# Performance work log

Measured on AMD Instinct MI355X. Metric: run time of the kernel, lower is better.

The kernel has to match this reference:

```python
import jax, jax.numpy as jnp
import numpy as np

DEPTH = 6
H = 12
D = 768
FF = 4 * D
OUT_INDICES = (2, 5)
EPS = 1e-5


def layernorm(x, g, b):
    m = jnp.mean(x, axis=-1, keepdims=True)
    v = jnp.mean(jnp.square(x - m), axis=-1, keepdims=True)
    return (x - m) * jax.lax.rsqrt(v + EPS) * g + b


def setup_inputs() -> dict:
    key = jax.random.key(0)
    ks = jax.random.split(key, 8)
    B, N = 2, 1024
    s = 0.02
    inp = {
        "x": jax.random.normal(ks[0], (B, N, D), dtype=jnp.float32),
        "rel_bias": jax.random.normal(ks[1], (H, N, N), dtype=jnp.float32),
        "ln1_g": jnp.ones((DEPTH, D), jnp.float32),
        "ln1_b": jnp.zeros((DEPTH, D), jnp.float32),
        "qkv_w": jax.random.normal(ks[2], (DEPTH, D, 3 * D), dtype=jnp.float32) * s,
        "out_w": jax.random.normal(ks[3], (DEPTH, D, D), dtype=jnp.float32) * s,
        "out_b": jnp.zeros((DEPTH, D), jnp.float32),
        "ln2_g": jnp.ones((DEPTH, D), jnp.float32),
        "ln2_b": jnp.zeros((DEPTH, D), jnp.float32),
        "ff1_w": jax.random.normal(ks[4], (DEPTH, D, FF), dtype=jnp.float32) * s,
        "ff1_b": jnp.zeros((DEPTH, FF), jnp.float32),
        "ff2_w": jax.random.normal(ks[5], (DEPTH, FF, D), dtype=jnp.float32) * s,
        "ff2_b": jnp.zeros((DEPTH, D), jnp.float32),
        "lnf_g": jnp.ones((D,), jnp.float32),
        "lnf_b": jnp.zeros((D,), jnp.float32),
    }
    return inp


def reference(x, rel_bias, ln1_g, ln1_b, qkv_w, out_w, out_b, ln2_g, ln2_b,
              ff1_w, ff1_b, ff2_w, ff2_b, lnf_g, lnf_b):
    B, N, Dm = x.shape
    Dh = Dm // H
    scale = Dh ** -0.5
    kside = int(round(N ** 0.5))  # N is a perfect square (patch grid)
    feats = []
    for i in range(DEPTH):
        # --- attention block ---
        h = layernorm(x, ln1_g[i], ln1_b[i])
        qkv = h @ qkv_w[i]                                   # [B,N,3D]
        q, k, v = jnp.split(qkv, 3, axis=-1)
        q = q.reshape(B, N, H, Dh).transpose(0, 2, 1, 3)     # [B,H,N,Dh]
        k = k.reshape(B, N, H, Dh).transpose(0, 2, 1, 3)
        v = v.reshape(B, N, H, Dh).transpose(0, 2, 1, 3)
        scores = jnp.einsum('bhid,bhjd->bhij', q, k) * scale + rel_bias
        attn = jax.nn.softmax(scores, axis=-1)
        o = jnp.einsum('bhij,bhjd->bhid', attn, v)
        o = o.transpose(0, 2, 1, 3).reshape(B, N, Dm)
        x = x + (o @ out_w[i] + out_b[i])
        # --- FFN block ---
        h2 = layernorm(x, ln2_g[i], ln2_b[i])
        ff = jax.nn.gelu(h2 @ ff1_w[i] + ff1_b[i], approximate=False)
        x = x + (ff @ ff2_w[i] + ff2_b[i])
        if i in OUT_INDICES:
            feats.append(x.reshape(B, kside, kside, Dm).transpose(0, 3, 1, 2))
    xf = layernorm(x, lnf_g, lnf_b)
    return (xf, *feats)
```

## Files before the change

### kernel.cpp

```cpp
#include <hip/hip_runtime.h>
#include <hip/hip_bf16.h>

typedef unsigned short ushort_t;
typedef __attribute__((ext_vector_type(8))) __bf16 bf16x8;
typedef __attribute__((ext_vector_type(4))) float f32x4;
typedef __attribute__((ext_vector_type(4))) unsigned int u32x4;

#define DEPTH 6
#define HEADS 12
#define DMODEL 768
#define FFDIM 3072
#define BATCH 2
#define SEQ 1024
#define ROWS (BATCH * SEQ)

static __device__ __forceinline__ ushort_t f2bf(float f) {
  unsigned u = __builtin_bit_cast(unsigned, f);
  u += 0x7fffu + ((u >> 16) & 1u);
  return (ushort_t)(u >> 16);
}

template <int MREP, int NREP, int EPI>
__global__ __launch_bounds__(256) void gemm_bt(
    const ushort_t* __restrict__ A, const ushort_t* __restrict__ Bt,
    int lda, int ldb, int K,
    void* __restrict__ out0, void* __restrict__ out1,
    const float* __restrict__ f0) {
  constexpr int BM = 32 * MREP;
  constexpr int BN = 32 * NREP;
  constexpr int CHA = BM / 32;
  constexpr int CHB = BN / 32;
  __shared__ ushort_t sA[2][BM * 64];
  __shared__ ushort_t sB[2][BN * 64];

  const int tid = threadIdx.x;
  const int lane = tid & 63;
  const int wid = tid >> 6;
  const int wm = wid >> 1, wn = wid & 1;

  const ushort_t* Ab = A + (long)blockIdx.x * BM * lda;
  const ushort_t* Bb = Bt + (long)blockIdx.y * BN * ldb;

  const int srow = lane >> 3;
  const int scol = ((lane & 7) ^ srow) * 8;

  f32x4 acc[MREP][NREP];
#pragma unroll
  for (int m = 0; m < MREP; ++m)
#pragma unroll
    for (int n = 0; n < NREP; ++n) acc[m][n] = (f32x4){0.f, 0.f, 0.f, 0.f};

  const int fr = lane & 15;
  const int kq4 = lane >> 4;

  auto stage_tile = [&](int buf, int t) {
    const int k0 = t * 64;
#pragma unroll
    for (int j = 0; j < CHA; ++j) {
      const int c = wid * CHA + j;
      const ushort_t* src = Ab + (long)(c * 8 + srow) * lda + k0 + scol;
      __builtin_amdgcn_global_load_lds(
          (const __attribute__((address_space(1))) void*)src,
          (__attribute__((address_space(3))) void*)&sA[buf][c * 512], 16, 0, 0);
    }
#pragma unroll
    for (int j = 0; j < CHB; ++j) {
      const int c = wid * CHB + j;
      const ushort_t* src = Bb + (long)(c * 8 + srow) * ldb + k0 + scol;
      __builtin_amdgcn_global_load_lds(
          (const __attribute__((address_space(1))) void*)src,
          (__attribute__((address_space(3))) void*)&sB[buf][c * 512], 16, 0, 0);
    }
  };

  const int nt = K / 64;
  stage_tile(0, 0);
  for (int t = 0; t < nt; ++t) {
    const int cur = t & 1;
    asm volatile("s_waitcnt vmcnt(0)" ::: "memory");
    __builtin_amdgcn_s_barrier();
    if (t + 1 < nt) stage_tile(cur ^ 1, t + 1);
#pragma unroll
    for (int kk = 0; kk < 2; ++kk) {
      bf16x8 af[MREP], bfr[NREP];
#pragma unroll
      for (int m = 0; m < MREP; ++m) {
        const int row = wm * (MREP * 16) + m * 16 + fr;
        const int ch = (kk * 4 + kq4) ^ (row & 7);
        af[m] = *(const bf16x8*)&sA[cur][row * 64 + ch * 8];
      }
#pragma unroll
      for (int n = 0; n < NREP; ++n) {
        const int row = wn * (NREP * 16) + n * 16 + fr;
        const int ch = (kk * 4 + kq4) ^ (row & 7);
        bfr[n] = *(const bf16x8*)&sB[cur][row * 64 + ch * 8];
      }
#pragma unroll
      for (int m = 0; m < MREP; ++m)
#pragma unroll
        for (int n = 0; n < NREP; ++n)
          acc[m][n] = __builtin_amdgcn_mfma_f32_16x16x32_bf16(
              af[m], bfr[n], acc[m][n], 0, 0, 0);
    }
  }

  const long grow0 = (long)blockIdx.x * BM + wm * (MREP * 16);
  const long gcol0 = (long)blockIdx.y * BN + wn * (NREP * 16);
  const int rr = (lane >> 4) * 4;
  const int cc = lane & 15;

#pragma unroll
  for (int m = 0; m < MREP; ++m) {
#pragma unroll
    for (int n = 0; n < NREP; ++n) {
#pragma unroll
      for (int r = 0; r < 4; ++r) {
        long row = grow0 + m * 16 + rr + r;
        long col = gcol0 + n * 16 + cc;
        float c = acc[m][n][r];
        if (EPI == 0) {
          ushort_t bv = f2bf(c);
          if (col < 1536) {
            ((ushort_t*)out0)[row * 2304 + col] = bv;
          } else {
            long h = (col - 1536) >> 6, d = (col - 1536) & 63;
            long b = row >> 10, i = row & 1023;
            ((ushort_t*)out1)[(((b * HEADS) + h) * 64 + d) * 1024 + i] = bv;
          }
        } else if (EPI == 3) {
          long idx = row * DMODEL + col;
          ((float*)out0)[idx] += c + f0[col];
        } else if (EPI == 4) {
          float t = c + f0[col];
          float g = 0.5f * t * (1.0f + erff(t * 0.70710678118f));
          ((ushort_t*)out0)[row * FFDIM + col] = f2bf(g);
        } else if (EPI == 5) {
          long idx = row * DMODEL + col;
          ((float*)out0)[idx] += c + f0[col];
        }
      }
    }
  }
}

__global__ __launch_bounds__(256) void flash_attn(
    const ushort_t* __restrict__ qkv,
    const ushort_t* __restrict__ vt,
    const float* __restrict__ rel,
    ushort_t* __restrict__ o) {
  __shared__ ushort_t sK[2][64 * 64];
  __shared__ ushort_t sV[2][64 * 64];
  __shared__ ushort_t sP[64 * 64];

  const int tid = threadIdx.x;
  const int lane = tid & 63;
  const int wid = tid >> 6;
  const int h = blockIdx.y, b = blockIdx.z;
  const int q0 = blockIdx.x * 64;

  const int fr = lane & 15;
  const int kq4 = lane >> 4;
  const int rr = kq4 * 4;
  const int cc = fr;

  const int srow = lane >> 3;
  const int scol = ((lane & 7) ^ srow) * 8;

  const ushort_t* qbase =
      qkv + (size_t)(b * 1024 + q0 + wid * 16 + fr) * 2304 + h * 64;
  bf16x8 qreg[2];
  qreg[0] = *(const bf16x8*)&qbase[kq4 * 8];
  qreg[1] = *(const bf16x8*)&qbase[32 + kq4 * 8];

  const ushort_t* Kbase = qkv + (size_t)(b * 1024) * 2304 + 768 + h * 64;
  const ushort_t* Vbase = vt + (size_t)((b * HEADS + h) * 64) * 1024;

  f32x4 acc_o[4];
  float m_run[4], l_run[4];
#pragma unroll
  for (int n = 0; n < 4; ++n) acc_o[n] = (f32x4){0.f, 0.f, 0.f, 0.f};
#pragma unroll
  for (int r = 0; r < 4; ++r) { m_run[r] = -1e30f; l_run[r] = 0.f; }

  auto stage_kv = [&](int buf, int t) {
#pragma unroll
    for (int j = 0; j < 2; ++j) {
      const int c = wid * 2 + j;
      const ushort_t* src = Kbase + (size_t)(t * 64 + c * 8 + srow) * 2304 + scol;
      __builtin_amdgcn_global_load_lds(
          (const __attribute__((address_space(1))) void*)src,
          (__attribute__((address_space(3))) void*)&sK[buf][c * 512], 16, 0, 0);
    }
#pragma unroll
    for (int j = 0; j < 2; ++j) {
      const int c = wid * 2 + j;
      const ushort_t* src = Vbase + (size_t)(c * 8 + srow) * 1024 + t * 64 + scol;
      __builtin_amdgcn_global_load_lds(
          (const __attribute__((address_space(1))) void*)src,
          (__attribute__((address_space(3))) void*)&sV[buf][c * 512], 16, 0, 0);
    }
  };

  stage_kv(0, 0);
  for (int t = 0; t < 16; ++t) {
    const int cur = t & 1;
    asm volatile("s_waitcnt vmcnt(0)" ::: "memory");
    __builtin_amdgcn_s_barrier();

    float bias[4][4];
    {
      const float* rb = rel + ((size_t)h << 20) +
                        (size_t)(q0 + wid * 16 + rr) * 1024 + t * 64 + cc;
#pragma unroll
      for (int n = 0; n < 4; ++n)
#pragma unroll
        for (int r = 0; r < 4; ++r) bias[n][r] = rb[(size_t)r * 1024 + n * 16];
    }

    if (t + 1 < 16) stage_kv(cur ^ 1, t + 1);

    f32x4 s[4];
#pragma unroll
    for (int n = 0; n < 4; ++n) s[n] = (f32x4){0.f, 0.f, 0.f, 0.f};
#pragma unroll
    for (int kk = 0; kk < 2; ++kk) {
#pragma unroll
      for (int n = 0; n < 4; ++n) {
        const int row = n * 16 + fr;
        const int ch = (kk * 4 + kq4) ^ (row & 7);
        bf16x8 kf = *(const bf16x8*)&sK[cur][row * 64 + ch * 8];
        s[n] =
            __builtin_amdgcn_mfma_f32_16x16x32_bf16(qreg[kk], kf, s[n], 0, 0, 0);
      }
    }

    float mr[4];
#pragma unroll
    for (int r = 0; r < 4; ++r) mr[r] = -1e30f;
#pragma unroll
    for (int n = 0; n < 4; ++n)
#pragma unroll
      for (int r = 0; r < 4; ++r) {
        float v = s[n][r] * 0.125f + bias[n][r];
        s[n][r] = v;
        mr[r] = fmaxf(mr[r], v);
      }
#pragma unroll
    for (int o_ = 1; o_ < 16; o_ <<= 1)
#pragma unroll
      for (int r = 0; r < 4; ++r) mr[r] = fmaxf(mr[r], __shfl_xor(mr[r], o_));

    float escale[4], psum[4];
#pragma unroll
    for (int r = 0; r < 4; ++r) {
      float mn = fmaxf(m_run[r], mr[r]);
      escale[r] = __expf(m_run[r] - mn);
      m_run[r] = mn;
      psum[r] = 0.f;
    }
#pragma unroll
    for (int n = 0; n < 4; ++n)
#pragma unroll
      for (int r = 0; r < 4; ++r) {
        float p = __expf(s[n][r] - m_run[r]);
        psum[r] += p;
        const int prow = wid * 16 + rr + r;
        const int pcol = n * 16 + cc;
        sP[prow * 64 + (((pcol >> 3) ^ (prow & 7)) << 3) + (pcol & 7)] = f2bf(p);
      }
#pragma unroll
    for (int o_ = 1; o_ < 16; o_ <<= 1)
#pragma unroll
      for (int r = 0; r < 4; ++r) psum[r] += __shfl_xor(psum[r], o_);
#pragma unroll
    for (int r = 0; r < 4; ++r) l_run[r] = l_run[r] * escale[r] + psum[r];

    asm volatile("s_waitcnt lgkmcnt(0)" ::: "memory");
    __builtin_amdgcn_s_barrier();

#pragma unroll
    for (int n = 0; n < 4; ++n)
#pragma unroll
      for (int r = 0; r < 4; ++r) acc_o[n][r] *= escale[r];
#pragma unroll
    for (int kk = 0; kk < 2; ++kk) {
      const int prow = wid * 16 + fr;
      const int pch = (kk * 4 + kq4) ^ (prow & 7);
      bf16x8 pf = *(const bf16x8*)&sP[prow * 64 + pch * 8];
#pragma unroll
      for (int n = 0; n < 4; ++n) {
        const int vrow = n * 16 + fr;
        const int vch = (kk * 4 + kq4) ^ (vrow & 7);
        bf16x8 vf = *(const bf16x8*)&sV[cur][vrow * 64 + vch * 8];
        acc_o[n] =
            __builtin_amdgcn_mfma_f32_16x16x32_bf16(pf, vf, acc_o[n], 0, 0, 0);
      }
    }
  }

  ushort_t* ob = o + (size_t)(b * 1024 + q0 + wid * 16) * 768 + h * 64;
#pragma unroll
  for (int r = 0; r < 4; ++r) {
    const float rinv = 1.f / l_run[r];
#pragma unroll
    for (int n = 0; n < 4; ++n)
      ob[(size_t)(rr + r) * 768 + n * 16 + cc] = f2bf(acc_o[n][r] * rinv);
  }
}

__global__ __launch_bounds__(256) void transpose_cast(
    const float* __restrict__ in, ushort_t* __restrict__ out, int R, int C) {
  __shared__ float t[32][33];
  const float* ip = in + (long)blockIdx.z * R * C;
  ushort_t* op = out + (long)blockIdx.z * R * C;
  int c0 = blockIdx.x * 32, r0 = blockIdx.y * 32;
  int tx = threadIdx.x;
  for (int i = threadIdx.y; i < 32; i += 8)
    t[i][tx] = ip[(long)(r0 + i) * C + c0 + tx];
  __syncthreads();
  for (int i = threadIdx.y; i < 32; i += 8)
    op[(long)(c0 + i) * R + r0 + tx] = f2bf(t[tx][i]);
}

__global__ __launch_bounds__(256) void ln_kernel(
    const float* __restrict__ x, const float* __restrict__ g,
    const float* __restrict__ b, void* __restrict__ out, int out_f32) {
  int row = blockIdx.x;
  int tid = threadIdx.x;
  int lane = tid & 63, wid = tid >> 6;
  const float* xr = x + (long)row * DMODEL;
  float v0 = xr[tid], v1 = xr[tid + 256], v2 = xr[tid + 512];
  float s = v0 + v1 + v2;
  __shared__ float red[8];
  for (int o = 32; o; o >>= 1) s += __shfl_xor(s, o);
  if (!lane) red[wid] = s;
  __syncthreads();
  float mean = (red[0] + red[1] + red[2] + red[3]) * (1.f / 768.f);
  float d0 = v0 - mean, d1 = v1 - mean, d2 = v2 - mean;
  float q = d0 * d0 + d1 * d1 + d2 * d2;
  for (int o = 32; o; o >>= 1) q += __shfl_xor(q, o);
  if (!lane) red[4 + wid] = q;
  __syncthreads();
  float var = (red[4] + red[5] + red[6] + red[7]) * (1.f / 768.f);
  float rs = rsqrtf(var + 1e-5f);
  float y0 = d0 * rs * g[tid] + b[tid];
  float y1 = d1 * rs * g[tid + 256] + b[tid + 256];
  float y2 = d2 * rs * g[tid + 512] + b[tid + 512];
  if (out_f32) {
    float* o_ = (float*)out + (long)row * DMODEL;
    o_[tid] = y0; o_[tid + 256] = y1; o_[tid + 512] = y2;
  } else {
    ushort_t* o_ = (ushort_t*)out + (long)row * DMODEL;
    o_[tid] = f2bf(y0); o_[tid + 256] = f2bf(y1); o_[tid + 512] = f2bf(y2);
  }
}

__global__ __launch_bounds__(256) void feat_kernel(const float* __restrict__ x,
                                                   float* __restrict__ out) {
  __shared__ float t[32][33];
  const float* xp = x + (long)blockIdx.z * SEQ * DMODEL;
  float* op = out + (long)blockIdx.z * DMODEL * SEQ;
  int n0 = blockIdx.x * 32, c0 = blockIdx.y * 32;
  int tx = threadIdx.x;
  for (int i = threadIdx.y; i < 32; i += 8)
    t[i][tx] = xp[(long)(n0 + i) * DMODEL + c0 + tx];
  __syncthreads();
  for (int i = threadIdx.y; i < 32; i += 8)
    op[(long)(c0 + i) * SEQ + n0 + tx] = t[tx][i];
}

extern "C" void kernel_launch(void* const* d_in, const int* in_sizes, int n_in,
                              void* d_out, int out_size, void* d_ws,
                              size_t ws_size, hipStream_t stream) {
  const float* x_in   = (const float*)d_in[0];
  const float* rel    = (const float*)d_in[1];
  const float* ln1_g  = (const float*)d_in[2];
  const float* ln1_b  = (const float*)d_in[3];
  const float* qkv_w  = (const float*)d_in[4];
  const float* out_w  = (const float*)d_in[5];
  const float* out_b  = (const float*)d_in[6];
  const float* ln2_g  = (const float*)d_in[7];
  const float* ln2_b  = (const float*)d_in[8];
  const float* ff1_w  = (const float*)d_in[9];
  const float* ff1_b  = (const float*)d_in[10];
  const float* ff2_w  = (const float*)d_in[11];
  const float* ff2_b  = (const float*)d_in[12];
  const float* lnf_g  = (const float*)d_in[13];
  const float* lnf_b  = (const float*)d_in[14];
  float* out = (float*)d_out;

  char* w = (char*)d_ws;
  ushort_t* wq_t = (ushort_t*)w; w += (size_t)DEPTH * 2304 * 768 * 2;
  ushort_t* wo_t = (ushort_t*)w; w += (size_t)DEPTH * 768 * 768 * 2;
  ushort_t* wf1_t = (ushort_t*)w; w += (size_t)DEPTH * 3072 * 768 * 2;
  ushort_t* wf2_t = (ushort_t*)w; w += (size_t)DEPTH * 768 * 3072 * 2;
  float* xb = (float*)w; w += (size_t)ROWS * DMODEL * 4;
  ushort_t* hb = (ushort_t*)w; w += (size_t)ROWS * DMODEL * 2;
  ushort_t* qkvb = (ushort_t*)w; w += (size_t)ROWS * 2304 * 2;
  ushort_t* vt = (ushort_t*)w; w += (size_t)BATCH * HEADS * 64 * 1024 * 2;
  ushort_t* ob = (ushort_t*)w; w += (size_t)ROWS * DMODEL * 2;
  ushort_t* ffb = (ushort_t*)w; w += (size_t)ROWS * FFDIM * 2;

  dim3 tb(32, 8);
  transpose_cast<<<dim3(2304 / 32, 768 / 32, DEPTH), tb, 0, stream>>>(
      qkv_w, wq_t, 768, 2304);
  transpose_cast<<<dim3(768 / 32, 768 / 32, DEPTH), tb, 0, stream>>>(
      out_w, wo_t, 768, 768);
  transpose_cast<<<dim3(3072 / 32, 768 / 32, DEPTH), tb, 0, stream>>>(
      ff1_w, wf1_t, 768, 3072);
  transpose_cast<<<dim3(768 / 32, 3072 / 32, DEPTH), tb, 0, stream>>>(
      ff2_w, wf2_t, 3072, 768);

  hipMemcpyAsync(xb, x_in, (size_t)ROWS * DMODEL * 4, hipMemcpyDeviceToDevice,
                 stream);

  for (int i = 0; i < DEPTH; ++i) {
    ln_kernel<<<ROWS, 256, 0, stream>>>(xb, ln1_g + i * 768, ln1_b + i * 768,
                                        hb, 0);
    gemm_bt<4, 4, 0><<<dim3(16, 18), 256, 0, stream>>>(
        hb, wq_t + (size_t)i * 2304 * 768, 768, 768, 768, qkvb, vt, nullptr);
    flash_attn<<<dim3(16, HEADS, BATCH), 256, 0, stream>>>(qkvb, vt, rel, ob);
    gemm_bt<4, 2, 3><<<dim3(16, 12), 256, 0, stream>>>(
        ob, wo_t + (size_t)i * 768 * 768, 768, 768, 768, xb, nullptr,
        out_b + i * 768);
    ln_kernel<<<ROWS, 256, 0, stream>>>(xb, ln2_g + i * 768, ln2_b + i * 768,
                                        hb, 0);
    gemm_bt<4, 4, 4><<<dim3(16, 24), 256, 0, stream>>>(
        hb, wf1_t + (size_t)i * 3072 * 768, 768, 768, 768, ffb, nullptr,
        ff1_b + i * 3072);
    gemm_bt<4, 2, 5><<<dim3(16, 12), 256, 0, stream>>>(
        ffb, wf2_t + (size_t)i * 768 * 3072, 3072, 3072, 3072, xb, nullptr,
        ff2_b + i * 768);
    if (i == 2)
      feat_kernel<<<dim3(32, 24, 2), tb, 0, stream>>>(xb, out + 1572864);
    if (i == 5)
      feat_kernel<<<dim3(32, 24, 2), tb, 0, stream>>>(xb, out + 2 * 1572864);
  }
  ln_kernel<<<ROWS, 256, 0, stream>>>(xb, lnf_g, lnf_b, out, 1);
}
```

Measured before the change: 991.2 us.

## Deepen GEMM pipeline to four K=32 stages and add grouped block swizzle

The bf16 MFMA GEMM now stages K tiles of 32 instead of 64 into a 4-deep LDS ring. Up to three tiles are in flight, using partial s_waitcnt vmcnt counts instead of draining all loads each iteration, which is meant to hide global-load latency. Block indices are also remapped with an 8-way interleave so that concurrently running blocks share A/B panels in cache. In exchange there are more barriers per unit of K, a new LDS swizzle pattern, and an assumption that the grid size divides by 8 and that MREP/NREP produce supported vmcnt values.

New measurement: 1.104 ms. +11.4%, slower.

```diff
diff --git a/kernel.cpp b/kernel.cpp
--- a/kernel.cpp
+++ b/kernel.cpp
@@ -18,6 +18,15 @@
   unsigned u = __builtin_bit_cast(unsigned, f);
   u += 0x7fffu + ((u >> 16) & 1u);
   return (ushort_t)(u >> 16);
+}
+
+template <int N>
+static __device__ __forceinline__ void wait_vmcnt() {
+  if constexpr (N == 0) asm volatile("s_waitcnt vmcnt(0)" ::: "memory");
+  else if constexpr (N == 3) asm volatile("s_waitcnt vmcnt(3)" ::: "memory");
+  else if constexpr (N == 4) asm volatile("s_waitcnt vmcnt(4)" ::: "memory");
+  else if constexpr (N == 6) asm volatile("s_waitcnt vmcnt(6)" ::: "memory");
+  else if constexpr (N == 8) asm volatile("s_waitcnt vmcnt(8)" ::: "memory");
 }
 
 template <int MREP, int NREP, int EPI>
@@ -28,21 +37,32 @@
     const float* __restrict__ f0) {
   constexpr int BM = 32 * MREP;
   constexpr int BN = 32 * NREP;
-  constexpr int CHA = BM / 32;
-  constexpr int CHB = BN / 32;
-  __shared__ ushort_t sA[2][BM * 64];
-  __shared__ ushort_t sB[2][BN * 64];
+  constexpr int CHA = BM / 64;
+  constexpr int CHB = BN / 64;
+  constexpr int L = CHA + CHB;
+  __shared__ ushort_t sA[4][BM * 32];
+  __shared__ ushort_t sB[4][BN * 32];
 
   const int tid = threadIdx.x;
   const int lane = tid & 63;
   const int wid = tid >> 6;
   const int wm = wid >> 1, wn = wid & 1;
 
-  const ushort_t* Ab = A + (long)blockIdx.x * BM * lda;
-  const ushort_t* Bb = Bt + (long)blockIdx.y * BN * ldb;
-
-  const int srow = lane >> 3;
-  const int scol = ((lane & 7) ^ srow) * 8;
+  int bx, by;
+  {
+    const int nb = gridDim.x * gridDim.y;
+    const int bid = blockIdx.y * gridDim.x + blockIdx.x;
+    const int q = nb >> 3;
+    const int swz = (bid & 7) * q + (bid >> 3);
+    bx = swz % gridDim.x;
+    by = swz / gridDim.x;
+  }
+
+  const ushort_t* Ab = A + (long)bx * BM * lda;
+  const ushort_t* Bb = Bt + (long)by * BN * ldb;
+
+  const int srow = lane >> 2;
+  const int scol = (((lane & 3) ^ ((lane >> 3) & 3))) * 8;
 
   f32x4 acc[MREP][NREP];
 #pragma unroll
@@ -54,11 +74,11 @@
   const int kq4 = lane >> 4;
 
   auto stage_tile = [&](int buf, int t) {
-    const int k0 = t * 64;
+    const int k0 = t * 32;
 #pragma unroll
     for (int j = 0; j < CHA; ++j) {
       const int c = wid * CHA + j;
-      const ushort_t* src = Ab + (long)(c * 8 + srow) * lda + k0 + scol;
+      const ushort_t* src = Ab + (long)(c * 16 + srow) * lda + k0 + scol;
       __builtin_amdgcn_global_load_lds(
           (const __attribute__((address_space(1))) void*)src,
           (__attribute__((address_space(3))) void*)&sA[buf][c * 512], 16, 0, 0);
@@ -66,46 +86,54 @@
 #pragma unroll
     for (int j = 0; j < CHB; ++j) {
       const int c = wid * CHB + j;
-      const ushort_t* src = Bb + (long)(c * 8 + srow) * ldb + k0 + scol;
+      const ushort_t* src = Bb + (long)(c * 16 + srow) * ldb + k0 + scol;
       __builtin_amdgcn_global_load_lds(
           (const __attribute__((address_space(1))) void*)src,
           (__attribute__((address_space(3))) void*)&sB[buf][c * 512], 16, 0, 0);
     }
   };
 
-  const int nt = K / 64;
+  auto compute_tile = [&](int buf) {
+    bf16x8 af[MREP], bfr[NREP];
+#pragma unroll
+    for (int m = 0; m < MREP; ++m) {
+      const int row = wm * (MREP * 16) + m * 16 + fr;
+      const int ch = kq4 ^ ((row >> 1) & 3);
+      af[m] = *(const bf16x8*)&sA[buf][row * 32 + ch * 8];
+    }
+#pragma unroll
+    for (int n = 0; n < NREP; ++n) {
+      const int row = wn * (NREP * 16) + n * 16 + fr;
+      const int ch = kq4 ^ ((row >> 1) & 3);
+      bfr[n] = *(const bf16x8*)&sB[buf][row * 32 + ch * 8];
+    }
+#pragma unroll
+    for (int m = 0; m < MREP; ++m)
+#pragma unroll
+      for (int n = 0; n < NREP; ++n)
+        acc[m][n] = __builtin_amdgcn_mfma_f32_16x16x32_bf16(
+            af[m], bfr[n], acc[m][n], 0, 0, 0);
+  };
+
+  const int nt = K / 32;
   stage_tile(0, 0);
-  for (int t = 0; t < nt; ++t) {
-    const int cur = t & 1;
-    asm volatile("s_waitcnt vmcnt(0)" ::: "memory");
+  stage_tile(1, 1);
+  stage_tile(2, 2);
+  for (int t = 0; t < nt - 2; ++t) {
+    wait_vmcnt<2 * L>();
     __builtin_amdgcn_s_barrier();
-    if (t + 1 < nt) stage_tile(cur ^ 1, t + 1);
-#pragma unroll
-    for (int kk = 0; kk < 2; ++kk) {
-      bf16x8 af[MREP], bfr[NREP];
-#pragma unroll
-      for (int m = 0; m < MREP; ++m) {
-        const int row = wm * (MREP * 16) + m * 16 + fr;
-        const int ch = (kk * 4 + kq4) ^ (row & 7);
-        af[m] = *(const bf16x8*)&sA[cur][row * 64 + ch * 8];
-      }
-#pragma unroll
-      for (int n = 0; n < NREP; ++n) {
-        const int row = wn * (NREP * 16) + n * 16 + fr;
-        const int ch = (kk * 4 + kq4) ^ (row & 7);
-        bfr[n] = *(const bf16x8*)&sB[cur][row * 64 + ch * 8];
-      }
-#pragma unroll
-      for (int m = 0; m < MREP; ++m)
-#pragma unroll
-        for (int n = 0; n < NREP; ++n)
-          acc[m][n] = __builtin_amdgcn_mfma_f32_16x16x32_bf16(
-              af[m], bfr[n], acc[m][n], 0, 0, 0);
-    }
-  }
-
-  const long grow0 = (long)blockIdx.x * BM + wm * (MREP * 16);
-  const long gcol0 = (long)blockIdx.y * BN + wn * (NREP * 16);
+    if (t + 3 < nt) stage_tile((t + 3) & 3, t + 3);
+    compute_tile(t & 3);
+  }
+  wait_vmcnt<L>();
+  __builtin_amdgcn_s_barrier();
+  compute_tile((nt - 2) & 3);
+  wait_vmcnt<0>();
+  __builtin_amdgcn_s_barrier();
+  compute_tile((nt - 1) & 3);
+
+  const long grow0 = (long)bx * BM + wm * (MREP * 16);
+  const long gcol0 = (long)by * BN + wn * (NREP * 16);
   const int rr = (lane >> 4) * 4;
   const int cc = lane & 15;
 
```
